# Performance work log

Hardware: AMD Instinct MI355X
Metric: run time of the kernel (lower is better)

## Reference

```python
import jax, jax.numpy as jnp
import numpy as np

K = 128      # num_topics
T = 256      # num_times
E = 320      # rho_size
H = 10       # num_heads (fixed in source)
HD = E // H  # head dim
TM1 = T - 1
EPS = 1e-5   # nn.LayerNorm default eps


def setup_inputs() -> dict:
    key = jax.random.key(0)
    ks = jax.random.split(key, 6)
    s = 0.02
    return {
        "mu_0_alpha": jax.random.normal(ks[0], (1, K, E), jnp.float32),
        "qkv_w": jax.random.normal(ks[1], (3 * E, E), jnp.float32) * s,
        "qkv_b": jnp.zeros((3 * E,), jnp.float32),
        "in_proj_w": jax.random.normal(ks[2], (3 * E, E), jnp.float32) * s,
        "in_proj_b": jnp.zeros((3 * E,), jnp.float32),
        "out_w": jax.random.normal(ks[3], (E, E), jnp.float32) * s,
        "out_b": jnp.zeros((E,), jnp.float32),
        "ln_g": jnp.ones((E,), jnp.float32),
        "ln_b": jnp.zeros((E,), jnp.float32),
    }


def _layer_norm(x, g, b):
    m = jnp.mean(x, axis=-1, keepdims=True)
    v = jnp.mean((x - m) ** 2, axis=-1, keepdims=True)
    return (x - m) * jax.lax.rsqrt(v + EPS) * g + b


def reference(mu_0_alpha, qkv_w, qkv_b, in_proj_w, in_proj_b, out_w, out_b, ln_g, ln_b):
    # nn.MultiheadAttention in-projection split (q/k/v same embed_dim)
    Wq, Wk, Wv = jnp.split(in_proj_w, 3, axis=0)   # each (E, E)
    bq, bk, bv = jnp.split(in_proj_b, 3, axis=0)
    scale = 1.0 / np.sqrt(HD)

    alpha0 = _layer_norm(mu_0_alpha[0], ln_g, ln_b)  # (K, E)
    kc0 = jnp.zeros((TM1 * K, E), jnp.float32)       # persistent projected-K cache
    vc0 = jnp.zeros((TM1 * K, E), jnp.float32)
    pos = jnp.arange(TM1 * K)

    def step(carry, idx):
        alpha, kc, vc = carry
        # per-step qkv_proj (the module's own Linear, before MHA's in-proj)
        qkv = alpha @ qkv_w.T + qkv_b                 # (K, 3E)
        q, k, v = jnp.split(qkv, 3, axis=-1)
        # MHA in-projections; store projected K/V in the cache (equivalent to
        # projecting the concatenated cache each step, since proj is per-row)
        q2 = (q @ Wq.T + bq) * scale                  # (K, E)
        k2 = k @ Wk.T + bk
        v2 = v @ Wv.T + bv
        kc = jax.lax.dynamic_update_slice(kc, k2, (idx * K, 0))
        vc = jax.lax.dynamic_update_slice(vc, v2, (idx * K, 0))
        qh = q2.reshape(K, H, HD).transpose(1, 0, 2)          # (H, K, HD)
        kh = kc.reshape(TM1 * K, H, HD).transpose(1, 0, 2)    # (H, S, HD)
        vh = vc.reshape(TM1 * K, H, HD).transpose(1, 0, 2)
        scores = jnp.einsum('hqd,hkd->hqk', qh, kh)           # (H, K, S)
        valid = pos < (idx + 1) * K                            # growing-KV mask
        scores = jnp.where(valid[None, None, :], scores, -1e30)
        w = jax.nn.softmax(scores, axis=-1)
        o = jnp.einsum('hqk,hkd->hqd', w, vh)                  # (H, K, HD)
        o = o.transpose(1, 0, 2).reshape(K, E) @ out_w.T + out_b
        new_alpha = _layer_norm(o + alpha, ln_g, ln_b)         # residual + LN
        return (new_alpha, kc, vc), new_alpha

    _, alphas_rest = jax.lax.scan(step, (alpha0, kc0, vc0), jnp.arange(TM1))
    return jnp.concatenate([alpha0[None], alphas_rest], axis=0)  # (T, K, E)
```

## Files before the change

### kernel.cpp

```cpp
#include <hip/hip_runtime.h>
#include <hip/hip_bf16.h>
#include <math.h>

typedef __hip_bfloat16 bf16;
using short4v = __attribute__((ext_vector_type(4))) short;
using short8 = __attribute__((ext_vector_type(8))) short;
using f32x4  = __attribute__((ext_vector_type(4))) float;

#define E_ 320
#define K_ 128
#define H_ 10
#define HD_ 32
#define T_ 256
#define TM1_ 255
#define SMAX_ (TM1_*K_)
#define MAXCH_ 30
#define QSCALE 0.17677669529663687f
#define EPS_LN 1e-5f

__device__ __forceinline__ float ldin(const void* p, size_t i, int isbf){
  if (isbf) return __bfloat162float(((const bf16*)p)[i]);
  return ((const float*)p)[i];
}
__device__ __forceinline__ void stout(void* p, size_t i, float v, int isbf){
  if (isbf) ((bf16*)p)[i] = __float2bfloat16(v);
  else      ((float*)p)[i] = v;
}

__device__ __forceinline__ void reduce2_320(float& a, float& b, float* sc){
  #pragma unroll
  for (int off = 32; off > 0; off >>= 1){
    a += __shfl_down(a, off, 64);
    b += __shfl_down(b, off, 64);
  }
  int w = threadIdx.x >> 6, lane = threadIdx.x & 63;
  __syncthreads();
  if (lane == 0){ sc[w] = a; sc[8+w] = b; }
  __syncthreads();
  a = sc[0]+sc[1]+sc[2]+sc[3]+sc[4];
  b = sc[8]+sc[9]+sc[10]+sc[11]+sc[12];
}

__global__ void detect_kernel(const void* __restrict__ mu0, int* __restrict__ flag){
  int lane = threadIdx.x;
  const unsigned short* u = (const unsigned short*)mu0;
  int cnt = 0;
  #pragma unroll
  for (int rep = 0; rep < 2; ++rep){
    unsigned short w = u[(size_t)(lane + rep*64) * 2];
    float v = __uint_as_float(((unsigned int)w) << 16);
    float a = fabsf(v);
    if (a >= 1e-4f && a <= 64.f) cnt++;
  }
  #pragma unroll
  for (int off = 32; off > 0; off >>= 1) cnt += __shfl_down(cnt, off, 64);
  if (lane == 0) *flag = (cnt >= 64) ? 1 : 0;
}

__global__ __launch_bounds__(256) void setup_wc(const void* __restrict__ inw,
                                                const void* __restrict__ qkvw,
                                                float* __restrict__ WcT,
                                                const int* __restrict__ flagp){
  const int isbf = *flagp;
  int sec = blockIdx.z;
  int i = blockIdx.y*16 + threadIdx.y;
  int o = blockIdx.x*16 + threadIdx.x;
  __shared__ float As[16][17];
  __shared__ float Bs[16][17];
  float acc = 0.f;
  for (int mt = 0; mt < E_; mt += 16){
    As[threadIdx.y][threadIdx.x] = ldin(inw, ((size_t)(sec*E_ + blockIdx.x*16 + threadIdx.x))*E_ + mt + threadIdx.y, isbf);
    Bs[threadIdx.y][threadIdx.x] = ldin(qkvw, ((size_t)(sec*E_ + mt + threadIdx.x))*E_ + blockIdx.y*16 + threadIdx.y, isbf);
    __syncthreads();
    #pragma unroll
    for (int mm = 0; mm < 16; ++mm) acc += Bs[threadIdx.y][mm] * As[mm][threadIdx.x];
    __syncthreads();
  }
  if (sec == 0) acc *= QSCALE;
  WcT[(size_t)i*960 + sec*E_ + o] = acc;
}

__global__ __launch_bounds__(256) void setup_misc(const void* __restrict__ inw,
                                                  const void* __restrict__ inb,
                                                  const void* __restrict__ qkvb,
                                                  const void* __restrict__ outw,
                                                  const void* __restrict__ outb,
                                                  const void* __restrict__ lng,
                                                  const void* __restrict__ lnb,
                                                  float* __restrict__ bc,
                                                  float* __restrict__ owT,
                                                  float* __restrict__ vec,
                                                  const int* __restrict__ flagp){
  const int isbf = *flagp;
  int id = blockIdx.x*256 + threadIdx.x;
  if (id < 960){
    int sec = id / E_, o = id % E_;
    float acc = 0.f;
    for (int m = 0; m < E_; ++m)
      acc += ldin(inw, ((size_t)(sec*E_+o))*E_ + m, isbf) * ldin(qkvb, sec*E_ + m, isbf);
    acc += ldin(inb, id, isbf);
    if (sec == 0) acc *= QSCALE;
    bc[id] = acc;
  }
  int j = id - 1024;
  if (j >= 0 && j < E_*E_){
    int i = j / E_, c = j % E_;
    owT[(size_t)i*E_ + c] = ldin(outw, (size_t)c*E_ + i, isbf);
  }
  int v = id - (1024 + E_*E_);
  if (v >= 0 && v < 960){
    if (v < 320)       vec[v] = ldin(outb, v, isbf);
    else if (v < 640)  vec[v] = ldin(lng, v - 320, isbf);
    else               vec[v] = ldin(lnb, v - 640, isbf);
  }
}

__global__ __launch_bounds__(320) void ln0_kernel(const void* __restrict__ mu0,
                                                  const float* __restrict__ vec,
                                                  float* __restrict__ alpha,
                                                  void* __restrict__ out,
                                                  const int* __restrict__ flagp){
  const int isbf = *flagp;
  int r = blockIdx.x, c = threadIdx.x;
  __shared__ float sc[16];
  float x = ldin(mu0, (size_t)r*E_ + c, isbf);
  float s = x, s2 = x*x;
  reduce2_320(s, s2, sc);
  float mean = s * (1.f/E_);
  float var  = s2 * (1.f/E_) - mean*mean;
  float y = (x - mean) * rsqrtf(var + EPS_LN) * vec[320 + c] + vec[640 + c];
  alpha[(size_t)r*E_ + c] = y;
  stout(out, (size_t)r*E_ + c, y, isbf);
}

__global__ __launch_bounds__(320) void project_kernel(const float* __restrict__ alpha,
                                                      const float* __restrict__ WcT,
                                                      const float* __restrict__ bc,
                                                      bf16* __restrict__ q2b,
                                                      bf16* __restrict__ kcb,
                                                      bf16* __restrict__ vtb,
                                                      int t){
  int c = blockIdx.x*320 + threadIdx.x;
  int r0 = blockIdx.y*4;
  __shared__ float sa[4][E_];
  #pragma unroll
  for (int j = 0; j < 4; ++j) sa[j][threadIdx.x] = alpha[(size_t)(r0+j)*E_ + threadIdx.x];
  __syncthreads();
  float a0=0.f, a1=0.f, a2=0.f, a3=0.f;
  for (int i = 0; i < E_; ++i){
    float w = WcT[(size_t)i*960 + c];
    a0 += sa[0][i]*w; a1 += sa[1][i]*w; a2 += sa[2][i]*w; a3 += sa[3][i]*w;
  }
  float bias = bc[c];
  float vals[4] = {a0+bias, a1+bias, a2+bias, a3+bias};
  if (c < E_){
    #pragma unroll
    for (int j = 0; j < 4; ++j) q2b[(size_t)(r0+j)*E_ + c] = __float2bfloat16(vals[j]);
  } else if (c < 2*E_){
    #pragma unroll
    for (int j = 0; j < 4; ++j) kcb[((size_t)(t*K_ + r0+j))*E_ + (c - E_)] = __float2bfloat16(vals[j]);
  } else {
    #pragma unroll
    for (int j = 0; j < 4; ++j) vtb[(size_t)(c - 2*E_)*SMAX_ + (size_t)t*K_ + r0+j] = __float2bfloat16(vals[j]);
  }
}

__global__ __launch_bounds__(512) void attn_mfma(const bf16* __restrict__ q2b,
                                                 const bf16* __restrict__ kcb,
                                                 const bf16* __restrict__ vtb,
                                                 float* __restrict__ part,
                                                 int S, int chunkS){
  int ci = blockIdx.x, h = blockIdx.y;
  int w    = threadIdx.x >> 6;
  int lane = threadIdx.x & 63;
  int cn   = lane & 15;
  int quad = lane >> 4;
  __shared__ bf16 pbuf[8][16][40];

  int s0 = ci*chunkS, s1 = min(s0 + chunkS, S);

  short8 qf = *(const short8*)(const void*)(q2b + (size_t)(w*16 + cn)*E_ + h*HD_ + quad*8);

  f32x4 accT[2];
  accT[0] = (f32x4){0.f,0.f,0.f,0.f};
  accT[1] = (f32x4){0.f,0.f,0.f,0.f};
  float mcol = -INFINITY, lcol = 0.f;

  for (int sb = s0; sb < s1; sb += 32){
    short8 kf0 = *(const short8*)(const void*)(kcb + (size_t)(sb +      cn)*E_ + h*HD_ + quad*8);
    short8 kf1 = *(const short8*)(const void*)(kcb + (size_t)(sb + 16 + cn)*E_ + h*HD_ + quad*8);
    short8 vf0 = *(const short8*)(const void*)(vtb + (size_t)(h*HD_ +      cn)*SMAX_ + sb + quad*8);
    short8 vf1 = *(const short8*)(const void*)(vtb + (size_t)(h*HD_ + 16 + cn)*SMAX_ + sb + quad*8);
    f32x4 z = (f32x4){0.f,0.f,0.f,0.f};
    f32x4 sT0 = __builtin_amdgcn_mfma_f32_16x16x32_bf16(kf0, qf, z, 0, 0, 0);
    f32x4 sT1 = __builtin_amdgcn_mfma_f32_16x16x32_bf16(kf1, qf, z, 0, 0, 0);

    float mx = fmaxf(fmaxf(fmaxf(sT0[0], sT0[1]), fmaxf(sT0[2], sT0[3])),
                     fmaxf(fmaxf(sT1[0], sT1[1]), fmaxf(sT1[2], sT1[3])));
    mx = fmaxf(mx, __shfl_xor(mx, 16, 64));
    mx = fmaxf(mx, __shfl_xor(mx, 32, 64));
    float mn = fmaxf(mcol, mx);
    float corr = __expf(mcol - mn);
    mcol = mn;

    float p0[4], p1[4];
    #pragma unroll
    for (int r = 0; r < 4; ++r){ p0[r] = __expf(sT0[r] - mn); p1[r] = __expf(sT1[r] - mn); }
    float ps = (p0[0]+p0[1]) + (p0[2]+p0[3]) + (p1[0]+p1[1]) + (p1[2]+p1[3]);
    ps += __shfl_xor(ps, 16, 64);
    ps += __shfl_xor(ps, 32, 64);
    lcol = lcol*corr + ps;
    accT[0] *= corr;
    accT[1] *= corr;

    union { short4v v; bf16 e[4]; } u0, u1;
    #pragma unroll
    for (int r = 0; r < 4; ++r){ u0.e[r] = __float2bfloat16(p0[r]); u1.e[r] = __float2bfloat16(p1[r]); }
    *(short4v*)(void*)(&pbuf[w][cn][quad*4])      = u0.v;
    *(short4v*)(void*)(&pbuf[w][cn][16 + quad*4]) = u1.v;
    asm volatile("s_waitcnt lgkmcnt(0)" ::: "memory");
    short8 pf = *(const short8*)(const void*)(&pbuf[w][cn][quad*8]);
    accT[0] = __builtin_amdgcn_mfma_f32_16x16x32_bf16(vf0, pf, accT[0], 0, 0, 0);
    accT[1] = __builtin_amdgcn_mfma_f32_16x16x32_bf16(vf1, pf, accT[1], 0, 0, 0);
  }

  size_t base = (((size_t)h*MAXCH_ + ci)*K_ + 16*w + cn)*36;
  *(f32x4*)(part + base + quad*4)      = accT[0];
  *(f32x4*)(part + base + 16 + quad*4) = accT[1];
  if (quad == 0){ part[base + 32] = mcol; part[base + 33] = lcol; }
}

__global__ __launch_bounds__(320) void combine_kernel(const float* __restrict__ part,
                                                      const float* __restrict__ owT,
                                                      const float* __restrict__ vec,
                                                      float* __restrict__ alpha,
                                                      void* __restrict__ out,
                                                      const int* __restrict__ flagp,
                                                      int t, int nch){
  const int isbf = *flagp;
  int tid = threadIdx.x;
  int r = blockIdx.x;
  int h = tid >> 5, d = tid & 31;
  __shared__ float s_att[E_];
  __shared__ float sc[16];
  float mstar = -INFINITY;
  for (int ci = 0; ci < nch; ++ci)
    mstar = fmaxf(mstar, part[(((size_t)h*MAXCH_ + ci)*K_ + r)*36 + 32]);
  float L = 0.f, acc = 0.f;
  for (int ci = 0; ci < nch; ++ci){
    size_t base = (((size_t)h*MAXCH_ + ci)*K_ + r)*36;
    float wgt = __expf(part[base+32] - mstar);
    L   += wgt * part[base+33];
    acc += wgt * part[base+d];
  }
  s_att[tid] = acc / L;
  __syncthreads();
  float a0 = vec[tid];
  for (int i = 0; i < E_; ++i) a0 += s_att[i]*owT[(size_t)i*E_ + tid];
  float g = vec[320 + tid];
  float bb = vec[640 + tid];
  float x = a0 + alpha[(size_t)r*E_ + tid];
  float s = x, s2 = x*x;
  reduce2_320(s, s2, sc);
  float mean = s * (1.f/E_);
  float var  = s2 * (1.f/E_) - mean*mean;
  float y = (x - mean) * rsqrtf(var + EPS_LN) * g + bb;
  alpha[(size_t)r*E_ + tid] = y;
  stout(out, ((size_t)(t+1)*K_ + r)*E_ + tid, y, isbf);
}

extern "C" void kernel_launch(void* const* d_in, const int* in_sizes, int n_in,
                              void* d_out, int out_size, void* d_ws, size_t ws_size,
                              hipStream_t stream){
  const void* mu0  = d_in[0];
  const void* qkvw = d_in[1];
  const void* qkvb = d_in[2];
  const void* inw  = d_in[3];
  const void* inb  = d_in[4];
  const void* outw = d_in[5];
  const void* outb = d_in[6];
  const void* lng  = d_in[7];
  const void* lnb  = d_in[8];
  float* ws = (float*)d_ws;

  const size_t O_WCT   = 0;
  const size_t O_BC    = 307200;
  const size_t O_OWT   = 308224;
  const size_t O_VEC   = 410624;
  const size_t O_ALPHA = 411648;
  const size_t O_PART  = 452608;
  const size_t O_FLAG  = 1835008;
  const size_t O_Q2    = 1835040;
  const size_t O_KC    = 1855520;
  const size_t O_VT    = 7077920;

  float* WcT   = ws + O_WCT;
  float* bc    = ws + O_BC;
  float* owT   = ws + O_OWT;
  float* vec   = ws + O_VEC;
  float* alpha = ws + O_ALPHA;
  float* part  = ws + O_PART;
  int*   flag  = (int*)(ws + O_FLAG);
  bf16*  q2b   = (bf16*)(ws + O_Q2);
  bf16*  kcb   = (bf16*)(ws + O_KC);
  bf16*  vtb   = (bf16*)(ws + O_VT);

  detect_kernel<<<dim3(1), dim3(64), 0, stream>>>(mu0, flag);
  setup_wc<<<dim3(20,20,3), dim3(16,16), 0, stream>>>(inw, qkvw, WcT, flag);
  setup_misc<<<dim3(408), dim3(256), 0, stream>>>(inw, inb, qkvb, outw, outb, lng, lnb, bc, owT, vec, flag);
  ln0_kernel<<<dim3(128), dim3(320), 0, stream>>>(mu0, vec, alpha, d_out, flag);

  for (int t = 0; t < TM1_; ++t){
    project_kernel<<<dim3(3,32), dim3(320), 0, stream>>>(alpha, WcT, bc, q2b, kcb, vtb, t);
    int S = (t+1)*K_;
    int nch = (S + 255) / 256; if (nch > MAXCH_) nch = MAXCH_;
    int chunkS = (((S + nch - 1)/nch) + 127) / 128 * 128;
    int nchU = (S + chunkS - 1) / chunkS;
    attn_mfma<<<dim3(nchU, H_), dim3(512), 0, stream>>>(q2b, kcb, vtb, part, S, chunkS);
    combine_kernel<<<dim3(128), dim3(320), 0, stream>>>(part, owT, vec, alpha, d_out, flag, t, nchU);
  }
}
```

Baseline: 19.16 ms.

## Fuse combine, out-proj, LayerNorm and next-step projection into one MFMA kernel

Merges the per-step combine kernel with the next step's projection kernel, cutting launches per step from three to two. Both GEMMs (out-projection and the fused QKV/in-projection) now use bf16 MFMA with bf16 weights instead of scalar fp32 loops. Alpha is double-buffered across steps because the three column-group blocks recompute the combine redundantly. Storing weights in bf16 lowers precision, and the combine work is repeated in each of the three column groups.

Measured after the change: 21.46 ms. 12.0% more time.

```diff
diff --git a/kernel.cpp b/kernel.cpp
--- a/kernel.cpp
+++ b/kernel.cpp
@@ -59,7 +59,7 @@
 
 __global__ __launch_bounds__(256) void setup_wc(const void* __restrict__ inw,
                                                 const void* __restrict__ qkvw,
-                                                float* __restrict__ WcT,
+                                                bf16* __restrict__ WcB,
                                                 const int* __restrict__ flagp){
   const int isbf = *flagp;
   int sec = blockIdx.z;
@@ -77,7 +77,7 @@
     __syncthreads();
   }
   if (sec == 0) acc *= QSCALE;
-  WcT[(size_t)i*960 + sec*E_ + o] = acc;
+  WcB[((size_t)(sec*E_ + o))*E_ + i] = __float2bfloat16(acc);
 }
 
 __global__ __launch_bounds__(256) void setup_misc(const void* __restrict__ inw,
@@ -88,7 +88,7 @@
                                                   const void* __restrict__ lng,
                                                   const void* __restrict__ lnb,
                                                   float* __restrict__ bc,
-                                                  float* __restrict__ owT,
+                                                  bf16* __restrict__ owB,
                                                   float* __restrict__ vec,
                                                   const int* __restrict__ flagp){
   const int isbf = *flagp;
@@ -104,8 +104,7 @@
   }
   int j = id - 1024;
   if (j >= 0 && j < E_*E_){
-    int i = j / E_, c = j % E_;
-    owT[(size_t)i*E_ + c] = ldin(outw, (size_t)c*E_ + i, isbf);
+    owB[j] = __float2bfloat16(ldin(outw, j, isbf));
   }
   int v = id - (1024 + E_*E_);
   if (v >= 0 && v < 960){
@@ -133,35 +132,140 @@
   stout(out, (size_t)r*E_ + c, y, isbf);
 }
 
-__global__ __launch_bounds__(320) void project_kernel(const float* __restrict__ alpha,
-                                                      const float* __restrict__ WcT,
-                                                      const float* __restrict__ bc,
-                                                      bf16* __restrict__ q2b,
-                                                      bf16* __restrict__ kcb,
-                                                      bf16* __restrict__ vtb,
-                                                      int t){
-  int c = blockIdx.x*320 + threadIdx.x;
-  int r0 = blockIdx.y*4;
-  __shared__ float sa[4][E_];
-  #pragma unroll
-  for (int j = 0; j < 4; ++j) sa[j][threadIdx.x] = alpha[(size_t)(r0+j)*E_ + threadIdx.x];
-  __syncthreads();
-  float a0=0.f, a1=0.f, a2=0.f, a3=0.f;
-  for (int i = 0; i < E_; ++i){
-    float w = WcT[(size_t)i*960 + c];
-    a0 += sa[0][i]*w; a1 += sa[1][i]*w; a2 += sa[2][i]*w; a3 += sa[3][i]*w;
-  }
-  float bias = bc[c];
-  float vals[4] = {a0+bias, a1+bias, a2+bias, a3+bias};
-  if (c < E_){
-    #pragma unroll
-    for (int j = 0; j < 4; ++j) q2b[(size_t)(r0+j)*E_ + c] = __float2bfloat16(vals[j]);
-  } else if (c < 2*E_){
-    #pragma unroll
-    for (int j = 0; j < 4; ++j) kcb[((size_t)(t*K_ + r0+j))*E_ + (c - E_)] = __float2bfloat16(vals[j]);
+__global__ __launch_bounds__(512) void cp_kernel(const float* __restrict__ part,
+                                                 const bf16* __restrict__ owB,
+                                                 const bf16* __restrict__ WcB,
+                                                 const float* __restrict__ bc,
+                                                 const float* __restrict__ vec,
+                                                 const float* __restrict__ ain,
+                                                 float* __restrict__ aout,
+                                                 void* __restrict__ out,
+                                                 const int* __restrict__ flagp,
+                                                 bf16* __restrict__ q2b,
+                                                 bf16* __restrict__ kcb,
+                                                 bf16* __restrict__ vtb,
+                                                 int t, int nch, int do_combine, int do_project){
+  const int isbf = *flagp;
+  int cg = blockIdx.x;
+  int rg = blockIdx.y;
+  int r0 = rg*16;
+  int tid = threadIdx.x;
+  int w = tid >> 6, lane = tid & 63, cn = lane & 15, quad = lane >> 4;
+
+  __shared__ bf16  af[16][328];
+  __shared__ float xbuf[16][328];
+  __shared__ bf16  a2[16][328];
+  __shared__ float mlw[16][10][MAXCH_];
+  __shared__ float mlL[16][10];
+
+  if (do_combine){
+    if (tid < 160){
+      int r = tid / 10, h = tid % 10;
+      float mst = -INFINITY;
+      for (int ci = 0; ci < nch; ++ci)
+        mst = fmaxf(mst, part[(((size_t)h*MAXCH_ + ci)*K_ + r0 + r)*36 + 32]);
+      float L = 0.f;
+      for (int ci = 0; ci < nch; ++ci){
+        size_t base = (((size_t)h*MAXCH_ + ci)*K_ + r0 + r)*36;
+        float wgt = __expf(part[base + 32] - mst);
+        mlw[r][h][ci] = wgt;
+        L += wgt * part[base + 33];
+      }
+      mlL[r][h] = L;
+    }
+    __syncthreads();
+    for (int v = tid; v < 16*E_; v += 512){
+      int r = v / E_, e = v % E_;
+      int h = e >> 5, d = e & 31;
+      float acc = 0.f;
+      for (int ci = 0; ci < nch; ++ci)
+        acc += mlw[r][h][ci] * part[(((size_t)h*MAXCH_ + ci)*K_ + r0 + r)*36 + d];
+      af[r][e] = __float2bfloat16(acc / mlL[r][h]);
+    }
+    __syncthreads();
+
+    {
+      f32x4 acc[3]; int ntv[3]; int ntc = 0;
+      for (int nt = w; nt < 20; nt += 8){ ntv[ntc] = nt; acc[ntc] = (f32x4){0.f,0.f,0.f,0.f}; ntc++; }
+      for (int kk = 0; kk < 10; ++kk){
+        short8 afr = *(const short8*)(const void*)(&af[cn][kk*32 + quad*8]);
+        for (int i = 0; i < ntc; ++i){
+          short8 bfr = *(const short8*)(const void*)(owB + ((size_t)(ntv[i]*16 + cn))*E_ + kk*32 + quad*8);
+          acc[i] = __builtin_amdgcn_mfma_f32_16x16x32_bf16(afr, bfr, acc[i], 0, 0, 0);
+        }
+      }
+      for (int i = 0; i < ntc; ++i){
+        int col = ntv[i]*16 + cn;
+        #pragma unroll
+        for (int rr = 0; rr < 4; ++rr){
+          int lr = quad*4 + rr;
+          xbuf[lr][col] = acc[i][rr] + vec[col] + ain[(size_t)(r0+lr)*E_ + col];
+        }
+      }
+    }
+    __syncthreads();
+
+    {
+      int lr = tid >> 5;
+      int j32 = tid & 31;
+      float s = 0.f, s2 = 0.f;
+      for (int c = j32; c < E_; c += 32){ float x = xbuf[lr][c]; s += x; s2 += x*x; }
+      #pragma unroll
+      for (int off = 1; off < 32; off <<= 1){
+        s  += __shfl_xor(s, off, 32);
+        s2 += __shfl_xor(s2, off, 32);
+      }
+      float mean = s * (1.f/E_);
+      float var  = s2 * (1.f/E_) - mean*mean;
+      float rs = rsqrtf(var + EPS_LN);
+      for (int c = j32; c < E_; c += 32){
+        float y = (xbuf[lr][c] - mean) * rs * vec[320 + c] + vec[640 + c];
+        a2[lr][c] = __float2bfloat16(y);
+        if (cg == 0){
+          aout[(size_t)(r0+lr)*E_ + c] = y;
+          stout(out, ((size_t)t*K_ + r0 + lr)*E_ + c, y, isbf);
+        }
+      }
+    }
+    __syncthreads();
   } else {
-    #pragma unroll
-    for (int j = 0; j < 4; ++j) vtb[(size_t)(c - 2*E_)*SMAX_ + (size_t)t*K_ + r0+j] = __float2bfloat16(vals[j]);
+    for (int v = tid; v < 16*E_; v += 512){
+      int r = v / E_, e = v % E_;
+      a2[r][e] = __float2bfloat16(ain[(size_t)(r0+r)*E_ + e]);
+    }
+    __syncthreads();
+  }
+
+  if (!do_project) return;
+
+  {
+    f32x4 acc[3]; int ntv[3]; int ntc = 0;
+    for (int nt = w; nt < 20; nt += 8){ ntv[ntc] = nt; acc[ntc] = (f32x4){0.f,0.f,0.f,0.f}; ntc++; }
+    for (int kk = 0; kk < 10; ++kk){
+      short8 afr = *(const short8*)(const void*)(&a2[cn][kk*32 + quad*8]);
+      for (int i = 0; i < ntc; ++i){
+        short8 bfr = *(const short8*)(const void*)(WcB + ((size_t)(cg*E_ + ntv[i]*16 + cn))*E_ + kk*32 + quad*8);
+        acc[i] = __builtin_amdgcn_mfma_f32_16x16x32_bf16(afr, bfr, acc[i], 0, 0, 0);
+      }
+    }
+    for (int i = 0; i < ntc; ++i){
+      int coll = ntv[i]*16 + cn;
+      float bias = bc[cg*E_ + coll];
+      if (cg == 0){
+        #pragma unroll
+        for (int rr = 0; rr < 4; ++rr)
+          q2b[(size_t)(r0 + quad*4 + rr)*E_ + coll] = __float2bfloat16(acc[i][rr] + bias);
+      } else if (cg == 1){
+        #pragma unroll
+        for (int rr = 0; rr < 4; ++rr)
+          kcb[((size_t)(t*K_ + r0 + quad*4 + rr))*E_ + coll] = __float2bfloat16(acc[i][rr] + bias);
+      } else {
+        union { short4v v; bf16 e[4]; } u;
+        #pragma unroll
+        for (int rr = 0; rr < 4; ++rr) u.e[rr] = __float2bfloat16(acc[i][rr] + bias);
+        *(short4v*)(void*)(vtb + (size_t)coll*SMAX_ + t*K_ + r0 + quad*4) = u.v;
+      }
+    }
   }
 }
 
@@ -228,45 +332,6 @@
   *(f32x4*)(part + base + quad*4)      = accT[0];
   *(f32x4*)(part + base + 16 + quad*4) = accT[1];
   if (quad == 0){ part[base + 32] = mcol; part[base + 33] = lcol; }
-}
-
-__global__ __launch_bounds__(320) void combine_kernel(const float* __restrict__ part,
-                                                      const float* __restrict__ owT,
-                                                      const float* __restrict__ vec,
-                                                      float* __restrict__ alpha,
-                                                      void* __restrict__ out,
-                                                      const int* __restrict__ flagp,
-                                                      int t, int nch){
-  const int isbf = *flagp;
-  int tid = threadIdx.x;
-  int r = blockIdx.x;
-  int h = tid >> 5, d = tid & 31;
-  __shared__ float s_att[E_];
-  __shared__ float sc[16];
-  float mstar = -INFINITY;
-  for (int ci = 0; ci < nch; ++ci)
-    mstar = fmaxf(mstar, part[(((size_t)h*MAXCH_ + ci)*K_ + r)*36 + 32]);
-  float L = 0.f, acc = 0.f;
-  for (int ci = 0; ci < nch; ++ci){
-    size_t base = (((size_t)h*MAXCH_ + ci)*K_ + r)*36;
-    float wgt = __expf(part[base+32] - mstar);
-    L   += wgt * part[base+33];
-    acc += wgt * part[base+d];
-  }
-  s_att[tid] = acc / L;
-  __syncthreads();
-  float a0 = vec[tid];
-  for (int i = 0; i < E_; ++i) a0 += s_att[i]*owT[(size_t)i*E_ + tid];
-  float g = vec[320 + tid];
-  float bb = vec[640 + tid];
-  float x = a0 + alpha[(size_t)r*E_ + tid];
-  float s = x, s2 = x*x;
-  reduce2_320(s, s2, sc);
-  float mean = s * (1.f/E_);
-  float var  = s2 * (1.f/E_) - mean*mean;
-  float y = (x - mean) * rsqrtf(var + EPS_LN) * g + bb;
-  alpha[(size_t)r*E_ + tid] = y;
-  stout(out, ((size_t)(t+1)*K_ + r)*E_ + tid, y, isbf);
 }
 
 extern "C" void kernel_launch(void* const* d_in, const int* in_sizes, int n_in,
@@ -283,22 +348,24 @@
   const void* lnb  = d_in[8];
   float* ws = (float*)d_ws;
 
-  const size_t O_WCT   = 0;
-  const size_t O_BC    = 307200;
-  const size_t O_OWT   = 308224;
-  const size_t O_VEC   = 410624;
-  const size_t O_ALPHA = 411648;
-  const size_t O_PART  = 452608;
-  const size_t O_FLAG  = 1835008;
-  const size_t O_Q2    = 1835040;
-  const size_t O_KC    = 1855520;
-  const size_t O_VT    = 7077920;
-
-  float* WcT   = ws + O_WCT;
+  const size_t O_WCB    = 0;
+  const size_t O_OWB    = 153600;
+  const size_t O_BC     = 204800;
+  const size_t O_VEC    = 205824;
+  const size_t O_ALPHA0 = 206848;
+  const size_t O_ALPHA1 = 247808;
+  const size_t O_PART   = 288768;
+  const size_t O_FLAG   = 1671168;
+  const size_t O_Q2     = 1671200;
+  const size_t O_KC     = 1691680;
+  const size_t O_VT     = 6914080;
+
+  bf16*  WcB   = (bf16*)(ws + O_WCB);
+  bf16*  owB   = (bf16*)(ws + O_OWB);
   float* bc    = ws + O_BC;
-  float* owT   = ws + O_OWT;
   float* vec   = ws + O_VEC;
-  float* alpha = ws + O_ALPHA;
+  float* abuf0 = ws + O_ALPHA0;
+  float* abuf1 = ws + O_ALPHA1;
   float* part  = ws + O_PART;
   int*   flag  = (int*)(ws + O_FLAG);
   bf16*  q2b   = (bf16*)(ws + O_Q2);
@@ -306,17 +373,30 @@
   bf16*  vtb   = (bf16*)(ws + O_VT);
 
   detect_kernel<<<dim3(1), dim3(64), 0, stream>>>(mu0, flag);
-  setup_wc<<<dim3(20,20,3), dim3(16,16), 0, stream>>>(inw, qkvw, WcT, flag);
-  setup_misc<<<dim3(408), dim3(256), 0, stream>>>(inw, inb, qkvb, outw, outb, lng, lnb, bc, owT, vec, flag);
-  ln0_kernel<<<dim3(128), dim3(320), 0, stream>>>(mu0, vec, alpha, d_out, flag);
-
+  setup_wc<<<dim3(20,20,3), dim3(16,16), 0, stream>>>(inw, qkvw, WcB, flag);
+  setup_misc<<<dim3(408), dim3(256), 0, stream>>>(inw, inb, qkvb, outw, outb, lng, lnb, bc, owB, vec, flag);
+  ln0_kernel<<<dim3(128), dim3(320), 0, stream>>>(mu0, vec, abuf0, d_out, flag);
+
+  int nch_prev = 0;
   for (int t = 0; t < TM1_; ++t){
-    project_kernel<<<dim3(3,32), dim3(320), 0, stream>>>(alpha, WcT, bc, q2b, kcb, vtb, t);
+    float* ain  = (t == 0) ? abuf0 : ((t & 1) ? abuf0 : abuf1);
+    float* aout = (t & 1) ? abuf1 : abuf0;
+    cp_kernel<<<dim3(3,8), dim3(512), 0, stream>>>(part, owB, WcB, bc, vec, ain, aout,
+                                                   d_out, flag, q2b, kcb, vtb,
+                                                   t, nch_prev, (t > 0) ? 1 : 0, 1);
     int S = (t+1)*K_;
     int nch = (S + 255) / 256; if (nch > MAXCH_) nch = MAXCH_;
     int chunkS = (((S + nch - 1)/nch) + 127) / 128 * 128;
     int nchU = (S + chunkS - 1) / chunkS;
     attn_mfma<<<dim3(nchU, H_), dim3(512), 0, stream>>>(q2b, kcb, vtb, part, S, chunkS);
-    combine_kernel<<<dim3(128), dim3(320), 0, stream>>>(part, owT, vec, alpha, d_out, flag, t, nchU);
-  }
-}
+    nch_prev = nchU;
+  }
+  {
+    int t = TM1_;
+    float* ain  = (t & 1) ? abuf0 : abuf1;
+    float* aout = (t & 1) ? abuf1 : abuf0;
+    cp_kernel<<<dim3(3,8), dim3(512), 0, stream>>>(part, owB, WcB, bc, vec, ain, aout,
+                                                   d_out, flag, q2b, kcb, vtb,
+                                                   t, nch_prev, 1, 0);
+  }
+}
```
